# Performance work log

Hardware: AMD Instinct MI355X
Metric: run time of the kernel (lower is better)

## Reference

```python
import jax, jax.numpy as jnp
import numpy as np

SMOOTH = 1.0      # self.smooth
NUM_ITER = 10     # iter_
EPS = 1e-07
INF = 1e12        # stand-in for +inf in squared-distance init


def _maxpool(x, window):
    # torch max_pool3d(stride=1, padding=w//2): pad with -inf, window max
    pads = ((0, 0), (0, 0)) + tuple((w // 2, w // 2) for w in window)
    return jax.lax.reduce_window(x, -jnp.inf, jax.lax.max, (1, 1) + window, (1, 1, 1, 1, 1), pads)


def _soft_erode(x):  # x: [B,1,D,H,W]
    p1 = -_maxpool(-x, (3, 1, 1))
    p2 = -_maxpool(-x, (1, 3, 1))
    p3 = -_maxpool(-x, (1, 1, 3))
    return jnp.minimum(jnp.minimum(p1, p2), p3)


def _soft_open(x):
    return _maxpool(_soft_erode(x), (3, 3, 3))  # dilate(erode(x))


def _soft_skel(x, n_iter):
    skel = jax.nn.relu(x - _soft_open(x))
    for _ in range(n_iter):
        x = _soft_erode(x)
        delta = jax.nn.relu(x - _soft_open(x))
        skel = skel + jax.nn.relu(delta - skel * delta)
    return skel


def _edt_pass(d2, axis):
    # 1D squared-distance min-convolution: out[i] = min_j (i-j)^2 + d2[j]
    L = d2.shape[axis]
    d2m = jnp.moveaxis(d2, axis, -1)                 # [..., L]
    i = jnp.arange(L, dtype=d2.dtype)
    sq = (i[:, None] - i[None, :]) ** 2              # [L, L]
    out = jnp.min(d2m[..., None, :] + sq, axis=-1)   # [..., L]
    return jnp.moveaxis(out, -1, axis)


def _edt(mask):
    # exact Euclidean distance transform: distance of nonzero voxels to nearest zero voxel
    d2 = jnp.where(mask > 0, INF, 0.0).astype(jnp.float32)  # [B,D,H,W]
    for ax in (1, 2, 3):
        d2 = _edt_pass(d2, ax)
    return jnp.sqrt(d2)


def _get_weights(mask, skel):
    # mask, skel: [B,D,H,W] binary float
    dist = _edt(mask)
    dist = jnp.where(mask == 0, 0.0, dist)
    on_skel = skel == 1
    skel_r = jnp.where(on_skel, dist, 0.0)
    rmax = jnp.max(skel_r.reshape(skel_r.shape[0], -1), axis=1).reshape(-1, 1, 1, 1)
    valid = rmax > 0
    rmax_safe = jnp.where(valid, rmax, 1.0)
    dist_n = jnp.where(valid, dist / rmax_safe, dist)
    skel_rn = jnp.where(valid, skel_r / rmax_safe, skel_r)
    # dim == 3 branch: skel_1_R2_norm
    skel_1r2 = jnp.where(on_skel, (1.0 + EPS) / (skel_rn ** 2 + EPS), 0.0)
    return dist_n, skel_rn, skel_1r2


def _combine(A, B, C):
    # D = B*C, overwritten by A*C where (A != 0) & (B == 0)
    return jnp.where((A != 0) & (B == 0), A * C, B * C)


def reference(y_pred, y_true):
    # y_pred: [B,C,D,H,W] logits; y_true: [B,1,D,H,W] int labels
    fore = jnp.max(y_pred[:, 1:], axis=1, keepdims=True)
    logits = jnp.concatenate([y_pred[:, :1], fore], axis=1)   # [B,2,D,H,W]
    prob = jax.nn.softmax(logits, axis=1)
    yp = (prob[:, 1] > 0.5).astype(jnp.float32)               # [B,D,H,W]
    yt = (y_true > 0).astype(jnp.float32)[:, 0]               # [B,D,H,W]

    skel_p = _soft_skel(yp[:, None], NUM_ITER)[:, 0]
    skel_t = _soft_skel(yt[:, None], NUM_ITER)[:, 0]

    q_vl, q_slvl, q_sl = _get_weights(yt, skel_t)
    q_vp, q_spvp, q_sp = _get_weights(yp, skel_p)

    w_tprec = (jnp.sum(q_sp * q_vl) + SMOOTH) / (jnp.sum(_combine(q_spvp, q_slvl, q_sp)) + SMOOTH)
    w_tsens = (jnp.sum(q_sl * q_vp) + SMOOTH) / (jnp.sum(_combine(q_slvl, q_spvp, q_sl)) + SMOOTH)
    return 1.0 - 2.0 * (w_tprec * w_tsens) / (w_tprec + w_tsens)


def setup_inputs() -> dict:
    key = jax.random.key(0)
    k1, k2 = jax.random.split(key)
    y_pred = jax.random.normal(k1, (2, 2, 64, 96, 96), dtype=jnp.float32)
    y_true = jax.random.randint(k2, (2, 1, 64, 96, 96), 0, 2, dtype=jnp.int32)
    return {"y_pred": y_pred, "y_true": y_true}
```

## Files before the change

kernel.cpp:

```cpp
#include <hip/hip_runtime.h>

namespace {

constexpr int Bn = 2;
constexpr int Dn = 64;
constexpr int Hn = 96;
constexpr int Wn = 96;
constexpr int HW = Hn * Wn;
constexpr int S  = Dn * HW;
constexpr int NBS = Bn * S;
constexpr int NT  = 2 * NBS;
constexpr int WPP = HW / 32;
constexpr int WPS = S / 32;
constexpr int NTW = NT / 32;
constexpr float EPSf = 1e-7f;
constexpr int BLK_SUMS = NBS / 4 / 256;
#define BIGF 1e12f

__global__ __launch_bounds__(256) void k_bin0(const float* __restrict__ logits,
                                              const int* __restrict__ labels,
                                              float* __restrict__ D2,
                                              unsigned char* __restrict__ D1z) {
  __shared__ unsigned bits[64];
  __shared__ unsigned zlo[32], zhi[32];
  int slab = blockIdx.x / 288;
  int cg = blockIdx.x - slab * 288;
  int c0 = cg * 32;
  int tid = threadIdx.x;
  int lane = tid & 63;
  for (int t = tid; t < 2048; t += 256) {
    int zz = t >> 5;
    int col = t & 31;
    int s = zz * HW + c0 + col;
    bool v;
    if (slab < 2) {
      float l0 = logits[(slab * 2 + 0) * S + s];
      float l1 = logits[(slab * 2 + 1) * S + s];
      v = l1 > l0;
    } else {
      v = labels[(slab - 2) * S + s] > 0;
    }
    unsigned long long m = __ballot(v);
    if (lane == 0)       bits[zz] = (unsigned)m;
    else if (lane == 32) bits[zz] = (unsigned)(m >> 32);
  }
  __syncthreads();
  if (tid < 64) {
    int col = tid & 31;
    int base = (tid < 32) ? 0 : 32;
    unsigned zw = 0u;
    #pragma unroll
    for (int j = 0; j < 32; ++j)
      zw |= (((bits[base + j] >> col) & 1u) ^ 1u) << j;
    if (tid < 32) zlo[col] = zw; else zhi[col] = zw;
  }
  __syncthreads();
  int col = tid & 31;
  int chunk = tid >> 5;
  int i0 = chunk * 8;
  unsigned long long Z = ((unsigned long long)zhi[col] << 32) | (unsigned long long)zlo[col];
  float* o = D2 + slab * S + c0 + col;
  unsigned char* o1 = D1z + slab * S + c0 + col;
  #pragma unroll
  for (int s = 0; s < 8; ++s) {
    int i = i0 + s;
    unsigned long long below = Z & ((2ull << i) - 1ull);
    unsigned long long above = Z >> i;
    float outv;
    int d1v;
    if (below | above) {
      int ddn = below ? (i - (63 - __builtin_clzll(below))) : 99;
      int dup = above ? __builtin_ctzll(above) : 99;
      int d = ddn < dup ? ddn : dup;
      outv = (float)(d * d);
      d1v = d < 13 ? d : 13;
    } else {
      outv = BIGF;
      d1v = 13;
    }
    o[i * HW] = outv;
    o1[i * HW] = (unsigned char)d1v;
  }
}

__global__ __launch_bounds__(192) void k_edtl1(const float* __restrict__ D2,
                                               const unsigned char* __restrict__ D1z,
                                               float* __restrict__ EF,
                                               unsigned char* __restrict__ D1) {
  __shared__ float Bh[24 * 97];
  __shared__ unsigned char L1b[24 * 96];
  int slab = blockIdx.x >> 8;
  int z = (blockIdx.x >> 2) & 63;
  int y0 = (blockIdx.x & 3) * 24;
  int tid = threadIdx.x;
  int pb = slab * S + z * HW;
  int xx = tid % 96;
  int c = tid / 96;
  int ybase = y0 + c * 12;
  {
    float m2[12];
    #pragma unroll
    for (int s = 0; s < 12; ++s) m2[s] = -2.0f * (float)(ybase + s);
    float best[12];
    #pragma unroll
    for (int s = 0; s < 12; ++s) best[s] = 3.4e38f;
    float jf = 0.0f;
    #pragma unroll 2
    for (int j = 0; j < Hn; ++j) {
      float f = D2[pb + j * 96 + xx];
      float g = fmaf(jf, jf, f);
      #pragma unroll
      for (int s = 0; s < 12; ++s)
        best[s] = fminf(best[s], fmaf(m2[s], jf, g));
      jf += 1.0f;
    }
    #pragma unroll
    for (int s = 0; s < 12; ++s) {
      float yf = (float)(ybase + s);
      Bh[(c * 12 + s) * 97 + xx] = fmaf(yf, yf, best[s]);
    }
  }
  {
    const unsigned char* dzc = D1z + pb + xx;
    int P = 255;
    for (int j = 0; j < ybase; ++j) P = min(P, (int)dzc[j * 96] - j);
    int A[12];
    #pragma unroll
    for (int s = 0; s < 12; ++s) {
      int j = ybase + s;
      P = min(P, (int)dzc[j * 96] - j);
      A[s] = j + P;
    }
    int Sv = 255;
    for (int j = 95; j >= ybase + 12; --j) Sv = min(Sv, (int)dzc[j * 96] + j);
    #pragma unroll
    for (int s = 11; s >= 0; --s) {
      int j = ybase + s;
      Sv = min(Sv, (int)dzc[j * 96] + j);
      int t1 = min(A[s], Sv - j);
      L1b[(c * 12 + s) * 96 + xx] = (unsigned char)(t1 < 13 ? t1 : 13);
    }
  }
  __syncthreads();
  int r = tid >> 3;
  int chunk = tid & 7;
  int i0 = chunk * 12;
  {
    float m2[12];
    #pragma unroll
    for (int s = 0; s < 12; ++s) m2[s] = -2.0f * (float)(i0 + s);
    float best[12];
    #pragma unroll
    for (int s = 0; s < 12; ++s) best[s] = 3.4e38f;
    float jf = 0.0f;
    #pragma unroll 2
    for (int j = 0; j < Wn; ++j) {
      float f = Bh[r * 97 + j];
      float g = fmaf(jf, jf, f);
      #pragma unroll
      for (int s = 0; s < 12; ++s)
        best[s] = fminf(best[s], fmaf(m2[s], jf, g));
      jf += 1.0f;
    }
    int gb = pb + (y0 + r) * 96 + i0;
    float outv[12];
    #pragma unroll
    for (int s = 0; s < 12; ++s) {
      float xf = (float)(i0 + s);
      outv[s] = fmaf(xf, xf, best[s]);
    }
    ((float4*)(EF + gb))[0] = make_float4(outv[0], outv[1], outv[2], outv[3]);
    ((float4*)(EF + gb))[1] = make_float4(outv[4], outv[5], outv[6], outv[7]);
    ((float4*)(EF + gb))[2] = make_float4(outv[8], outv[9], outv[10], outv[11]);
  }
  {
    const unsigned char* row = &L1b[r * 96];
    int P = 255;
    for (int j = 0; j < i0; ++j) P = min(P, (int)row[j] - j);
    int A[12];
    #pragma unroll
    for (int s = 0; s < 12; ++s) {
      int j = i0 + s;
      P = min(P, (int)row[j] - j);
      A[s] = j + P;
    }
    int Sv = 255;
    for (int j = 95; j >= i0 + 12; --j) Sv = min(Sv, (int)row[j] + j);
    unsigned dv[3] = {0u, 0u, 0u};
    #pragma unroll
    for (int s = 11; s >= 0; --s) {
      int j = i0 + s;
      Sv = min(Sv, (int)row[j] + j);
      int d1 = min(A[s], Sv - j);
      d1 = d1 < 12 ? d1 : 12;
      dv[s >> 2] |= ((unsigned)d1) << ((s & 3) * 8);
    }
    unsigned* dst = (unsigned*)(D1 + pb + (y0 + r) * 96 + i0);
    dst[0] = dv[0]; dst[1] = dv[1]; dst[2] = dv[2];
  }
}

__global__ __launch_bounds__(256) void k_skelmax(const unsigned char* __restrict__ D1,
                                                 const float* __restrict__ EF,
                                                 unsigned* __restrict__ SKELB,
                                                 float* __restrict__ pmax) {
  __shared__ unsigned char zm[26 * 96];
  __shared__ unsigned char cen[26 * 96];
  __shared__ float ldsf[4];
  int slab = blockIdx.x >> 8;
  int z = (blockIdx.x >> 2) & 63;
  int y0 = (blockIdx.x & 3) * 24;
  int tid = threadIdx.x;
  int pb = slab * S + z * HW;
  for (int t = tid; t < 2496; t += 256) {
    int rr = t / 96;
    int x = t - rr * 96;
    int yy = y0 - 1 + rr;
    unsigned char m = 0, cv = 0;
    if (yy >= 0 && yy < Hn) {
      int base = slab * S + yy * 96 + x;
      cv = D1[base + z * HW];
      m = cv;
      if (z > 0) { unsigned char a = D1[base + (z - 1) * HW]; m = m > a ? m : a; }
      if (z < Dn - 1) { unsigned char a = D1[base + (z + 1) * HW]; m = m > a ? m : a; }
    }
    zm[t] = m;
    cen[t] = cv;
  }
  __syncthreads();
  float mm = 0.0f;
  int wbase = slab * WPS + z * WPP + y0 * 3;
  int lane = tid & 63;
  #pragma unroll
  for (int round = 0; round < 9; ++round) {
    int v = round * 256 + tid;
    int rr = v / 96;
    int x = v - rr * 96;
    int b1 = rr * 96 + x;
    unsigned char mx = zm[b1];
    { unsigned char a = zm[b1 + 96]; mx = mx > a ? mx : a; }
    { unsigned char a = zm[b1 + 192]; mx = mx > a ? mx : a; }
    if (x > 0) {
      unsigned char a0 = zm[b1 - 1], a1 = zm[b1 + 95], a2 = zm[b1 + 191];
      unsigned char a = a0 > a1 ? a0 : a1; a = a > a2 ? a : a2;
      mx = mx > a ? mx : a;
    }
    if (x < Wn - 1) {
      unsigned char a0 = zm[b1 + 1], a1 = zm[b1 + 97], a2 = zm[b1 + 193];
      unsigned char a = a0 > a1 ? a0 : a1; a = a > a2 ? a : a2;
      mx = mx > a ? mx : a;
    }
    unsigned char d1 = cen[b1 + 96];
    bool sk = (d1 == mx) && (d1 >= 1) && (d1 <= 11);
    unsigned long long bal = __ballot(sk);
    if (lane == 0)       SKELB[wbase + (v >> 5)] = (unsigned)bal;
    else if (lane == 32) SKELB[wbase + (v >> 5)] = (unsigned)(bal >> 32);
    if (sk) mm = fmaxf(mm, EF[pb + (y0 + rr) * 96 + x]);
  }
  #pragma unroll
  for (int o = 32; o > 0; o >>= 1) mm = fmaxf(mm, __shfl_xor(mm, o, 64));
  if (lane == 0) ldsf[tid >> 6] = mm;
  __syncthreads();
  if (tid == 0)
    pmax[blockIdx.x] = fmaxf(fmaxf(ldsf[0], ldsf[1]), fmaxf(ldsf[2], ldsf[3]));
}

__global__ __launch_bounds__(256) void k_sums(const float* __restrict__ d2,
                                              const unsigned* __restrict__ skel,
                                              const float* __restrict__ pmax,
                                              double* __restrict__ ps) {
  __shared__ float lmax[4];
  __shared__ double ldsd[4][4];
  int tid = threadIdx.x;
  {
    int wave = tid >> 6, lane = tid & 63;
    const float* pw = pmax + wave * 256;
    float v = fmaxf(fmaxf(pw[lane], pw[lane + 64]),
                    fmaxf(pw[lane + 128], pw[lane + 192]));
    #pragma unroll
    for (int o = 32; o > 0; o >>= 1) v = fmaxf(v, __shfl_xor(v, o, 64));
    if (lane == 0) lmax[wave] = v;
  }
  __syncthreads();
  int q = blockIdx.x * 256 + tid;
  int idx0 = q * 4;
  int b = idx0 / S;
  float rmax_p = sqrtf(lmax[b]);
  float rmax_t = sqrtf(lmax[2 + b]);
  float4 dp4 = ((const float4*)d2)[q];
  float4 dt4 = ((const float4*)(d2 + NBS))[q];
  unsigned spw = (skel[idx0 >> 5] >> (idx0 & 31)) & 0xFu;
  unsigned stw = (skel[(NBS + idx0) >> 5] >> (idx0 & 31)) & 0xFu;
  const float* dp = &dp4.x;
  const float* dt = &dt4.x;
  double acc[4] = {0.0, 0.0, 0.0, 0.0};
  #pragma unroll
  for (int s = 0; s < 4; ++s) {
    float dist_p = sqrtf(dp[s]);
    float dist_t = sqrtf(dt[s]);
    bool sp = (spw >> s) & 1u;
    bool st = (stw >> s) & 1u;
    float q_vp = (rmax_p > 0.0f) ? dist_p / rmax_p : dist_p;
    float q_vl = (rmax_t > 0.0f) ? dist_t / rmax_t : dist_t;
    float q_spvp = sp ? q_vp : 0.0f;
    float q_slvl = st ? q_vl : 0.0f;
    float q_sp = sp ? (1.0f + EPSf) / (q_spvp * q_spvp + EPSf) : 0.0f;
    float q_sl = st ? (1.0f + EPSf) / (q_slvl * q_slvl + EPSf) : 0.0f;
    acc[0] += (double)(q_sp * q_vl);
    acc[1] += (double)(((q_spvp != 0.0f) && (q_slvl == 0.0f)) ? q_spvp * q_sp
                                                              : q_slvl * q_sp);
    acc[2] += (double)(q_sl * q_vp);
    acc[3] += (double)(((q_slvl != 0.0f) && (q_spvp == 0.0f)) ? q_slvl * q_sl
                                                              : q_spvp * q_sl);
  }
  #pragma unroll
  for (int k = 0; k < 4; ++k)
    #pragma unroll
    for (int o = 32; o > 0; o >>= 1)
      acc[k] += __shfl_xor(acc[k], o, 64);
  if ((tid & 63) == 0) {
    #pragma unroll
    for (int k = 0; k < 4; ++k) ldsd[tid >> 6][k] = acc[k];
  }
  __syncthreads();
  if (tid == 0) {
    #pragma unroll
    for (int k = 0; k < 4; ++k)
      ps[blockIdx.x * 4 + k] = ldsd[0][k] + ldsd[1][k] + ldsd[2][k] + ldsd[3][k];
  }
}

__global__ __launch_bounds__(256) void k_final(const double* __restrict__ ps,
                                               float* __restrict__ out) {
  __shared__ double ldsd[4][4];
  int tid = threadIdx.x;
  double s[4] = {0.0, 0.0, 0.0, 0.0};
  for (int i = tid; i < BLK_SUMS; i += 256) {
    s[0] += ps[i * 4 + 0];
    s[1] += ps[i * 4 + 1];
    s[2] += ps[i * 4 + 2];
    s[3] += ps[i * 4 + 3];
  }
  #pragma unroll
  for (int k = 0; k < 4; ++k)
    #pragma unroll
    for (int o = 32; o > 0; o >>= 1)
      s[k] += __shfl_xor(s[k], o, 64);
  if ((tid & 63) == 0) {
    #pragma unroll
    for (int k = 0; k < 4; ++k) ldsd[tid >> 6][k] = s[k];
  }
  __syncthreads();
  if (tid == 0) {
    double tot[4];
    #pragma unroll
    for (int k = 0; k < 4; ++k)
      tot[k] = ldsd[0][k] + ldsd[1][k] + ldsd[2][k] + ldsd[3][k];
    double wp = (tot[0] + 1.0) / (tot[1] + 1.0);
    double ws = (tot[2] + 1.0) / (tot[3] + 1.0);
    out[0] = (float)(1.0 - 2.0 * (wp * ws) / (wp + ws));
  }
}

}

extern "C" void kernel_launch(void* const* d_in, const int* in_sizes, int n_in,
                              void* d_out, int out_size, void* d_ws, size_t ws_size,
                              hipStream_t stream) {
  (void)in_sizes; (void)n_in; (void)out_size; (void)ws_size;
  const float* logits = (const float*)d_in[0];
  const int* labels   = (const int*)d_in[1];
  float* out = (float*)d_out;

  float* EF = (float*)d_ws;
  float* D2 = EF + NT;
  unsigned char* D1z = (unsigned char*)(D2 + NT);
  unsigned char* D1  = D1z + NT;
  unsigned* SKELB = (unsigned*)(D1 + NT);
  float* PMAX  = (float*)(SKELB + NTW);
  double* PS   = (double*)(PMAX + 1024);

  k_bin0<<<1152, 256, 0, stream>>>(logits, labels, D2, D1z);
  k_edtl1<<<1024, 192, 0, stream>>>(D2, D1z, EF, D1);
  k_skelmax<<<1024, 256, 0, stream>>>(D1, EF, SKELB, PMAX);
  k_sums<<<1152, 256, 0, stream>>>(EF, SKELB, PMAX, PS);
  k_final<<<1, 256, 0, stream>>>(PS, out);
}
```

Baseline: 143.4 us.

## Bound EDT min-convolution windows by L1 distance and compact intermediates to u16/u8

The Y and X passes of the distance transform no longer scan all 96 candidates per voxel. They use the already computed L1 (chamfer) distance as a search radius, since the exact squared Euclidean distance cannot come from farther away than that. Intermediates shrink from float to 16-bit squared distances and 8-bit distances, and each z-plane is staged into LDS with vector loads. The price is data-dependent loop lengths that cause wave divergence, and serial row scans run by only a few threads, which may cost parallelism. The 16-bit encoding also relies on the squared distances staying below 65535.

After: 118.6 us. 17.3% less time.

```diff
diff --git a/kernel.cpp b/kernel.cpp
--- a/kernel.cpp
+++ b/kernel.cpp
@@ -16,11 +16,12 @@
 constexpr float EPSf = 1e-7f;
 constexpr int BLK_SUMS = NBS / 4 / 256;
 #define BIGF 1e12f
+constexpr int LINF = 1 << 20;
 
 __global__ __launch_bounds__(256) void k_bin0(const float* __restrict__ logits,
                                               const int* __restrict__ labels,
-                                              float* __restrict__ D2,
-                                              unsigned char* __restrict__ D1z) {
+                                              unsigned short* __restrict__ FZ,
+                                              unsigned char* __restrict__ DZ) {
   __shared__ unsigned bits[64];
   __shared__ unsigned zlo[32], zhi[32];
   int slab = blockIdx.x / 288;
@@ -59,144 +60,156 @@
   int chunk = tid >> 5;
   int i0 = chunk * 8;
   unsigned long long Z = ((unsigned long long)zhi[col] << 32) | (unsigned long long)zlo[col];
-  float* o = D2 + slab * S + c0 + col;
-  unsigned char* o1 = D1z + slab * S + c0 + col;
+  unsigned short* o = FZ + slab * S + c0 + col;
+  unsigned char* o1 = DZ + slab * S + c0 + col;
   #pragma unroll
   for (int s = 0; s < 8; ++s) {
     int i = i0 + s;
     unsigned long long below = Z & ((2ull << i) - 1ull);
     unsigned long long above = Z >> i;
-    float outv;
-    int d1v;
+    unsigned short fv;
+    unsigned char dv;
     if (below | above) {
       int ddn = below ? (i - (63 - __builtin_clzll(below))) : 99;
       int dup = above ? __builtin_ctzll(above) : 99;
       int d = ddn < dup ? ddn : dup;
-      outv = (float)(d * d);
-      d1v = d < 13 ? d : 13;
+      fv = (unsigned short)(d * d);
+      dv = (unsigned char)d;
     } else {
-      outv = BIGF;
-      d1v = 13;
-    }
-    o[i * HW] = outv;
-    o1[i * HW] = (unsigned char)d1v;
-  }
-}
-
-__global__ __launch_bounds__(192) void k_edtl1(const float* __restrict__ D2,
-                                               const unsigned char* __restrict__ D1z,
+      fv = 0xFFFFu;
+      dv = 255;
+    }
+    o[i * HW] = fv;
+    o1[i * HW] = dv;
+  }
+}
+
+__global__ __launch_bounds__(256) void k_edtl1(const unsigned short* __restrict__ FZ,
+                                               const unsigned char* __restrict__ DZ,
                                                float* __restrict__ EF,
                                                unsigned char* __restrict__ D1) {
-  __shared__ float Bh[24 * 97];
-  __shared__ unsigned char L1b[24 * 96];
+  __shared__ __align__(16) unsigned shm[8640];
+  unsigned short* fz = (unsigned short*)shm;
+  unsigned char*  dz = (unsigned char*)(shm + 4608);
+  unsigned char*  t1 = (unsigned char*)(shm + 6912);
+  unsigned short* o1 = (unsigned short*)(shm + 7488);
+  unsigned short* Afwd = (unsigned short*)shm;
+  unsigned short* Bbwd = (unsigned short*)(shm + 4608);
   int slab = blockIdx.x >> 8;
   int z = (blockIdx.x >> 2) & 63;
   int y0 = (blockIdx.x & 3) * 24;
   int tid = threadIdx.x;
   int pb = slab * S + z * HW;
-  int xx = tid % 96;
-  int c = tid / 96;
-  int ybase = y0 + c * 12;
   {
-    float m2[12];
-    #pragma unroll
-    for (int s = 0; s < 12; ++s) m2[s] = -2.0f * (float)(ybase + s);
-    float best[12];
-    #pragma unroll
-    for (int s = 0; s < 12; ++s) best[s] = 3.4e38f;
-    float jf = 0.0f;
-    #pragma unroll 2
-    for (int j = 0; j < Hn; ++j) {
-      float f = D2[pb + j * 96 + xx];
-      float g = fmaf(jf, jf, f);
-      #pragma unroll
-      for (int s = 0; s < 12; ++s)
-        best[s] = fminf(best[s], fmaf(m2[s], jf, g));
-      jf += 1.0f;
-    }
-    #pragma unroll
-    for (int s = 0; s < 12; ++s) {
-      float yf = (float)(ybase + s);
-      Bh[(c * 12 + s) * 97 + xx] = fmaf(yf, yf, best[s]);
-    }
-  }
-  {
-    const unsigned char* dzc = D1z + pb + xx;
-    int P = 255;
-    for (int j = 0; j < ybase; ++j) P = min(P, (int)dzc[j * 96] - j);
-    int A[12];
-    #pragma unroll
-    for (int s = 0; s < 12; ++s) {
-      int j = ybase + s;
-      P = min(P, (int)dzc[j * 96] - j);
+    const uint4* s4 = (const uint4*)(FZ + pb);
+    uint4* d4 = (uint4*)fz;
+    for (int t = tid; t < 1152; t += 256) d4[t] = s4[t];
+    const uint4* s2 = (const uint4*)(DZ + pb);
+    uint4* d2 = (uint4*)(shm + 4608);
+    for (int t = tid; t < 576; t += 256) d2[t] = s2[t];
+  }
+  __syncthreads();
+  if (tid < 96) {
+    int xx = tid;
+    int P = LINF;
+    int A[24];
+    for (int j = 0; j < y0; ++j) {
+      int v = dz[j * 96 + xx]; if (v == 255) v = LINF;
+      P = min(P, v - j);
+    }
+    #pragma unroll
+    for (int s = 0; s < 24; ++s) {
+      int j = y0 + s;
+      int v = dz[j * 96 + xx]; if (v == 255) v = LINF;
+      P = min(P, v - j);
       A[s] = j + P;
     }
-    int Sv = 255;
-    for (int j = 95; j >= ybase + 12; --j) Sv = min(Sv, (int)dzc[j * 96] + j);
-    #pragma unroll
-    for (int s = 11; s >= 0; --s) {
-      int j = ybase + s;
-      Sv = min(Sv, (int)dzc[j * 96] + j);
-      int t1 = min(A[s], Sv - j);
-      L1b[(c * 12 + s) * 96 + xx] = (unsigned char)(t1 < 13 ? t1 : 13);
-    }
-  }
-  __syncthreads();
-  int r = tid >> 3;
-  int chunk = tid & 7;
-  int i0 = chunk * 12;
-  {
-    float m2[12];
-    #pragma unroll
-    for (int s = 0; s < 12; ++s) m2[s] = -2.0f * (float)(i0 + s);
-    float best[12];
-    #pragma unroll
-    for (int s = 0; s < 12; ++s) best[s] = 3.4e38f;
-    float jf = 0.0f;
-    #pragma unroll 2
-    for (int j = 0; j < Wn; ++j) {
-      float f = Bh[r * 97 + j];
-      float g = fmaf(jf, jf, f);
-      #pragma unroll
-      for (int s = 0; s < 12; ++s)
-        best[s] = fminf(best[s], fmaf(m2[s], jf, g));
-      jf += 1.0f;
-    }
-    int gb = pb + (y0 + r) * 96 + i0;
-    float outv[12];
-    #pragma unroll
-    for (int s = 0; s < 12; ++s) {
-      float xf = (float)(i0 + s);
-      outv[s] = fmaf(xf, xf, best[s]);
-    }
-    ((float4*)(EF + gb))[0] = make_float4(outv[0], outv[1], outv[2], outv[3]);
-    ((float4*)(EF + gb))[1] = make_float4(outv[4], outv[5], outv[6], outv[7]);
-    ((float4*)(EF + gb))[2] = make_float4(outv[8], outv[9], outv[10], outv[11]);
-  }
-  {
-    const unsigned char* row = &L1b[r * 96];
-    int P = 255;
-    for (int j = 0; j < i0; ++j) P = min(P, (int)row[j] - j);
-    int A[12];
-    #pragma unroll
-    for (int s = 0; s < 12; ++s) {
-      int j = i0 + s;
-      P = min(P, (int)row[j] - j);
-      A[s] = j + P;
-    }
-    int Sv = 255;
-    for (int j = 95; j >= i0 + 12; --j) Sv = min(Sv, (int)row[j] + j);
-    unsigned dv[3] = {0u, 0u, 0u};
-    #pragma unroll
-    for (int s = 11; s >= 0; --s) {
-      int j = i0 + s;
-      Sv = min(Sv, (int)row[j] + j);
-      int d1 = min(A[s], Sv - j);
-      d1 = d1 < 12 ? d1 : 12;
-      dv[s >> 2] |= ((unsigned)d1) << ((s & 3) * 8);
-    }
-    unsigned* dst = (unsigned*)(D1 + pb + (y0 + r) * 96 + i0);
-    dst[0] = dv[0]; dst[1] = dv[1]; dst[2] = dv[2];
+    int Sv = LINF;
+    for (int j = 95; j >= y0 + 24; --j) {
+      int v = dz[j * 96 + xx]; if (v == 255) v = LINF;
+      Sv = min(Sv, v + j);
+    }
+    #pragma unroll
+    for (int s = 23; s >= 0; --s) {
+      int j = y0 + s;
+      int v = dz[j * 96 + xx]; if (v == 255) v = LINF;
+      Sv = min(Sv, v + j);
+      int t = min(A[s], Sv - j);
+      t1[s * 96 + xx] = (unsigned char)(t > 254 ? 255 : t);
+    }
+  }
+  __syncthreads();
+  for (int v = tid; v < 2304; v += 256) {
+    int rr = v / 96;
+    int xx = v - rr * 96;
+    int y = y0 + rr;
+    int r = t1[rr * 96 + xx];
+    unsigned short res;
+    if (r == 255) {
+      res = 0xFFFFu;
+    } else {
+      int lo = y - r; if (lo < 0) lo = 0;
+      int hi = y + r; if (hi > 95) hi = 95;
+      int best = 1 << 30;
+      for (int j = lo; j <= hi; ++j) {
+        unsigned short f = fz[j * 96 + xx];
+        if (f != 0xFFFFu) {
+          int dd = y - j;
+          best = min(best, dd * dd + (int)f);
+        }
+      }
+      res = (unsigned short)best;
+    }
+    o1[rr * 96 + xx] = res;
+  }
+  __syncthreads();
+  if (tid < 24) {
+    int rr = tid;
+    int P = LINF;
+    for (int j = 0; j < 96; ++j) {
+      int v = t1[rr * 96 + j]; if (v == 255) v = LINF;
+      P = min(P, v - j);
+      int a = j + P;
+      Afwd[rr * 96 + j] = (unsigned short)(a > 60000 ? 60000 : a);
+    }
+  }
+  if (tid >= 64 && tid < 88) {
+    int rr = tid - 64;
+    int Sv = LINF;
+    for (int j = 95; j >= 0; --j) {
+      int v = t1[rr * 96 + j]; if (v == 255) v = LINF;
+      Sv = min(Sv, v + j);
+      int b = Sv - j;
+      Bbwd[rr * 96 + j] = (unsigned short)(b > 60000 ? 60000 : b);
+    }
+  }
+  __syncthreads();
+  for (int v = tid; v < 2304; v += 256) {
+    int rr = v / 96;
+    int x = v - rr * 96;
+    int d1v = min((int)Afwd[rr * 96 + x], (int)Bbwd[rr * 96 + x]);
+    float outf;
+    int d1c;
+    if (d1v > 253) {
+      outf = BIGF;
+      d1c = 12;
+    } else {
+      d1c = d1v < 12 ? d1v : 12;
+      int lo = x - d1v; if (lo < 0) lo = 0;
+      int hi = x + d1v; if (hi > 95) hi = 95;
+      int best = 1 << 30;
+      for (int j = lo; j <= hi; ++j) {
+        unsigned short f = o1[rr * 96 + j];
+        if (f != 0xFFFFu) {
+          int dd = x - j;
+          best = min(best, dd * dd + (int)f);
+        }
+      }
+      outf = (float)best;
+    }
+    int gb = pb + (y0 + rr) * 96 + x;
+    EF[gb] = outf;
+    D1[gb] = (unsigned char)d1c;
   }
 }
 
@@ -373,15 +386,15 @@
   float* out = (float*)d_out;
 
   float* EF = (float*)d_ws;
-  float* D2 = EF + NT;
-  unsigned char* D1z = (unsigned char*)(D2 + NT);
-  unsigned char* D1  = D1z + NT;
+  unsigned short* FZ = (unsigned short*)(EF + NT);
+  unsigned char* DZ  = (unsigned char*)(FZ + NT);
+  unsigned char* D1  = DZ + NT;
   unsigned* SKELB = (unsigned*)(D1 + NT);
   float* PMAX  = (float*)(SKELB + NTW);
   double* PS   = (double*)(PMAX + 1024);
 
-  k_bin0<<<1152, 256, 0, stream>>>(logits, labels, D2, D1z);
-  k_edtl1<<<1024, 192, 0, stream>>>(D2, D1z, EF, D1);
+  k_bin0<<<1152, 256, 0, stream>>>(logits, labels, FZ, DZ);
+  k_edtl1<<<1024, 256, 0, stream>>>(FZ, DZ, EF, D1);
   k_skelmax<<<1024, 256, 0, stream>>>(D1, EF, SKELB, PMAX);
   k_sums<<<1152, 256, 0, stream>>>(EF, SKELB, PMAX, PS);
   k_final<<<1, 256, 0, stream>>>(PS, out);
```
